# Kernel optimization log

Hardware: AMD Instinct MI355X
Metric: run time of the kernel (lower is better)

Reference implementation:

```python
import jax, jax.numpy as jnp
import numpy as np

N, C, H, W = 16, 256, 48, 96
S = 64   # num_s = 2*num_state_mid; also num_n = mids*mids = 64 (must match)
EPS = 1e-5


def setup_inputs() -> dict:
    key = jax.random.key(0)
    ks = jax.random.split(key, 11)
    sc = 0.05
    return {
        "x": jax.random.normal(ks[0], (N, C, H, W), jnp.float32),
        "edge": jax.random.normal(ks[1], (N, 2, H, W), jnp.float32),
        # conv_state: Conv2d(C, S, 1) with bias
        "Ws": jax.random.normal(ks[2], (S, C), jnp.float32) * sc,
        "bs": jax.random.normal(ks[3], (S,), jnp.float32) * sc,
        # conv_proj: Conv2d(C, S, 1) with bias
        "Wp": jax.random.normal(ks[4], (S, C), jnp.float32) * sc,
        "bp": jax.random.normal(ks[5], (S,), jnp.float32) * sc,
        # GCN conv1: Conv1d(num_n, num_n, 1, bias=False)
        "W1": jax.random.normal(ks[6], (S, S), jnp.float32) * sc,
        # GCN conv2: Conv1d(S, S, 1, bias=False)
        "W2": jax.random.normal(ks[7], (S, S), jnp.float32) * sc,
        # conv_extend: Conv2d(S, C, 1, bias=False)
        "We": jax.random.normal(ks[8], (C, S), jnp.float32) * sc,
        # BatchNorm2d(C) affine params (training-mode batch stats used in forward)
        "gamma": jnp.ones((C,), jnp.float32),
        "beta": jnp.zeros((C,), jnp.float32),
    }


def reference(x, edge, Ws, bs, Wp, bp, W1, W2, We, gamma, beta):
    n, c, h, w = x.shape
    s = Ws.shape[0]
    # edge softmax over channels, take class-1 probability map  -> (n,1,h,w)
    edge_g = jax.nn.softmax(edge, axis=1)[:, 1:2]

    # 1x1 convs as channel matmuls
    xs = jnp.einsum('oc,nchw->nohw', Ws, x) + bs[None, :, None, None]
    xs = xs.reshape(n, s, h * w)                        # (n,S,HW)
    xp = jnp.einsum('oc,nchw->nohw', Wp, x) + bp[None, :, None, None]
    # x_proj_region + x_proj_edge == xp * (1 + edge_gate)
    comb = (xp * (1.0 + edge_g)).reshape(n, s, h * w)
    comb = jax.nn.softmax(comb, axis=-1)                # softmax over spatial

    # project to graph space: (n,S,HW) @ (n,HW,S) -> (n,S,S)
    xn = jnp.einsum('nsk,ntk->nst', xs, comb)

    # GCN: conv1 over node dim (last axis mixes via W1), subtract, conv2 over state dim, relu
    hh = jnp.einsum('ij,nsj->nsi', W1, xn) - xn
    hh = jax.nn.relu(jnp.einsum('ij,njk->nik', W2, hh))

    # back-project: (n,S,S) @ (n,S,HW) -> (n,S,HW) -> (n,S,H,W)
    xr = jnp.einsum('nst,ntk->nsk', hh, comb).reshape(n, s, h, w)

    # conv_extend (no bias) then BatchNorm2d in training mode (biased batch var)
    ext = jnp.einsum('os,nshw->nohw', We, xr)
    mean = ext.mean(axis=(0, 2, 3), keepdims=True)
    var = ext.var(axis=(0, 2, 3), keepdims=True)
    bn = gamma[None, :, None, None] * (ext - mean) * jax.lax.rsqrt(var + EPS) \
         + beta[None, :, None, None]
    return x + bn
```

## Files before the change

### kernel.cpp

```cpp
#include <hip/hip_runtime.h>

#define HW 4608
#define NB 16
#define CC 256
#define SS 64
#define EPS 1e-5f
#define NSPLIT 24

typedef __attribute__((ext_vector_type(8))) short short8;
typedef __attribute__((ext_vector_type(4))) float f32x4;

__device__ __forceinline__ ushort f2bf(float f) {
    uint u = __float_as_uint(f);
    return (ushort)((u + 0x7FFFu + ((u >> 16) & 1u)) >> 16);
}
__device__ __forceinline__ float bf2f(ushort h) {
    return __uint_as_float(((uint)h) << 16);
}

__global__ __launch_bounds__(256) void k_wf(const float* __restrict__ Ws,
                                            const float* __restrict__ Wp,
                                            ushort* __restrict__ Wf) {
    int idx = blockIdx.x * 256 + threadIdx.x;
    int j = idx & 7, r = (idx >> 3) & 127, kq = (idx >> 10) & 3, cs = idx >> 12;
    int c = cs * 32 + kq * 8 + j;
    float v = (r < 64) ? Ws[r * CC + c] : Wp[(r - 64) * CC + c];
    Wf[idx] = f2bf(v);
}

__global__ __launch_bounds__(256) void k_proj(const float* __restrict__ x,
                                              const ushort* __restrict__ Wf,
                                              const float* __restrict__ bs,
                                              const float* __restrict__ bp,
                                              const float* __restrict__ edge,
                                              ushort* __restrict__ xsb,
                                              ushort* __restrict__ Eb,
                                              float* __restrict__ rsum) {
    __shared__ __align__(16) ushort Bl[32 * 64 * 8];
    int n = blockIdx.y, k0 = blockIdx.x * 64;
    int tid = threadIdx.x, lane = tid & 63, w = tid >> 6;
    int q = lane >> 4, li = lane & 15;
    const float* xb = x + (size_t)n * CC * HW + k0 + lane;
#pragma unroll
    for (int i = 0; i < 8; i++) {
        int kq = i * 4 + w;
        union { ushort u[8]; uint4 v; } tmp;
#pragma unroll
        for (int j = 0; j < 8; j++)
            tmp.u[j] = f2bf(xb[(size_t)(kq * 8 + j) * HW]);
        *(uint4*)&Bl[(kq * 64 + lane) * 8] = tmp.v;
    }
    __syncthreads();
    f32x4 acc[2][4] = {};
    uint4 afn[2];
#pragma unroll
    for (int mt = 0; mt < 2; mt++)
        afn[mt] = *(const uint4*)&Wf[((0 * 4 + q) * 128 + w * 32 + mt * 16 + li) * 8];
#pragma unroll
    for (int cs = 0; cs < 8; cs++) {
        short8 af[2];
        af[0] = *(short8*)&afn[0];
        af[1] = *(short8*)&afn[1];
        if (cs < 7) {
#pragma unroll
            for (int mt = 0; mt < 2; mt++)
                afn[mt] = *(const uint4*)&Wf[(((cs + 1) * 4 + q) * 128 + w * 32 + mt * 16 + li) * 8];
        }
        short8 bfr[4];
#pragma unroll
        for (int nt = 0; nt < 4; nt++) {
            uint4 t = *(const uint4*)&Bl[((cs * 4 + q) * 64 + nt * 16 + li) * 8];
            bfr[nt] = *(short8*)&t;
        }
#pragma unroll
        for (int mt = 0; mt < 2; mt++)
#pragma unroll
            for (int nt = 0; nt < 4; nt++)
                acc[mt][nt] = __builtin_amdgcn_mfma_f32_16x16x32_bf16(af[mt], bfr[nt], acc[mt][nt], 0, 0, 0);
    }
    if (w < 2) {
#pragma unroll
        for (int mt = 0; mt < 2; mt++) {
#pragma unroll
            for (int rr = 0; rr < 4; rr++) {
                int s = w * 32 + mt * 16 + q * 4 + rr;
                float bv = bs[s];
#pragma unroll
                for (int nt = 0; nt < 4; nt++) {
                    int col = k0 + nt * 16 + li;
                    xsb[((size_t)n * SS + s) * HW + col] = f2bf(acc[mt][nt][rr] + bv);
                }
            }
        }
    } else {
        float ga[4];
#pragma unroll
        for (int nt = 0; nt < 4; nt++) {
            int col = k0 + nt * 16 + li;
            float e0 = edge[((size_t)n * 2 + 0) * HW + col];
            float e1 = edge[((size_t)n * 2 + 1) * HW + col];
            ga[nt] = 1.f + 1.f / (1.f + __expf(e0 - e1));
        }
        float rp[2][4];
#pragma unroll
        for (int mt = 0; mt < 2; mt++) {
#pragma unroll
            for (int rr = 0; rr < 4; rr++) {
                int s = (w - 2) * 32 + mt * 16 + q * 4 + rr;
                float bv = bp[s];
                float sum = 0.f;
#pragma unroll
                for (int nt = 0; nt < 4; nt++) {
                    int col = k0 + nt * 16 + li;
                    float e = __expf((acc[mt][nt][rr] + bv) * ga[nt]);
                    sum += e;
                    Eb[((size_t)n * SS + s) * HW + col] = f2bf(e);
                }
                rp[mt][rr] = sum;
            }
        }
#pragma unroll
        for (int b = 1; b < 16; b <<= 1)
#pragma unroll
            for (int mt = 0; mt < 2; mt++)
#pragma unroll
                for (int rr = 0; rr < 4; rr++)
                    rp[mt][rr] += __shfl_xor(rp[mt][rr], b, 64);
        if (li == 0) {
#pragma unroll
            for (int mt = 0; mt < 2; mt++)
#pragma unroll
                for (int rr = 0; rr < 4; rr++)
                    atomicAdd(&rsum[n * SS + (w - 2) * 32 + mt * 16 + q * 4 + rr], rp[mt][rr]);
        }
    }
}

__global__ __launch_bounds__(256) void k_graph(const ushort* __restrict__ xsb,
                                               const ushort* __restrict__ Eb,
                                               float* __restrict__ Up,
                                               float* __restrict__ Pp) {
    int n = blockIdx.y, sp = blockIdx.x;
    int kbase = sp * (HW / NSPLIT);
    int tid = threadIdx.x, lane = tid & 63, w = tid >> 6;
    int q = lane >> 4, li = lane & 15;
    bool isP = w >= 2;
    int half = w & 1;
    const ushort* Arow = isP ? Eb : xsb;
    f32x4 acc[2][4] = {};
    for (int ks = 0; ks < (HW / NSPLIT) / 32; ks++) {
        int kb = kbase + ks * 32 + q * 8;
        short8 af[2], bfr[4];
#pragma unroll
        for (int mt = 0; mt < 2; mt++) {
            int s = half * 32 + mt * 16 + li;
            uint4 t = *(const uint4*)&Arow[((size_t)n * SS + s) * HW + kb];
            af[mt] = *(short8*)&t;
        }
#pragma unroll
        for (int nt = 0; nt < 4; nt++) {
            int tt = nt * 16 + li;
            uint4 t = *(const uint4*)&Eb[((size_t)n * SS + tt) * HW + kb];
            bfr[nt] = *(short8*)&t;
        }
#pragma unroll
        for (int mt = 0; mt < 2; mt++)
#pragma unroll
            for (int nt = 0; nt < 4; nt++)
                acc[mt][nt] = __builtin_amdgcn_mfma_f32_16x16x32_bf16(af[mt], bfr[nt], acc[mt][nt], 0, 0, 0);
    }
    float* dst = (isP ? Pp : Up) + ((size_t)sp * NB + n) * 4096;
#pragma unroll
    for (int mt = 0; mt < 2; mt++)
#pragma unroll
        for (int nt = 0; nt < 4; nt++)
#pragma unroll
            for (int rr = 0; rr < 4; rr++) {
                int row = half * 32 + mt * 16 + q * 4 + rr;
                int col = nt * 16 + li;
                dst[row * 64 + col] = acc[mt][nt][rr];
            }
}

__global__ __launch_bounds__(256) void k_red(const float* __restrict__ Up,
                                             const float* __restrict__ Pp,
                                             float* __restrict__ U,
                                             float* __restrict__ P) {
    int idx = blockIdx.x * 256 + threadIdx.x;
    const float* src = (idx < 16384) ? Up : Pp;
    float* dst = (idx < 16384) ? U : P;
    int o = (idx & 16383) * 4;
    f32x4 s = {};
    for (int sp = 0; sp < NSPLIT; sp++) {
        f32x4 v = *(const f32x4*)&src[(size_t)sp * 65536 + o];
        s += v;
    }
    *(f32x4*)&dst[o] = s;
}

__global__ __launch_bounds__(256) void k_gcn(const float* __restrict__ U,
                                             const float* __restrict__ rsum,
                                             const float* __restrict__ W1,
                                             const float* __restrict__ W2,
                                             const float* __restrict__ We,
                                             float* __restrict__ M,
                                             ushort* __restrict__ Mf) {
    __shared__ __align__(16) float A[64 * 68];
    __shared__ __align__(16) float B[64 * 68];
    __shared__ __align__(16) float Cb[64 * 68];
    __shared__ float rs[64];
    int n = blockIdx.x;
    int cc = blockIdx.y;
    int tid = threadIdx.x;
    int t0 = tid >> 4, t1 = tid & 15;
    if (tid < 64) rs[tid] = 1.0f / rsum[n * SS + tid];
    __syncthreads();
#pragma unroll
    for (int i = 0; i < 16; i++) {
        int idx = tid + i * 256;
        int r = idx >> 6, cth = idx & 63;
        A[cth * 68 + r] = U[n * 4096 + idx] * rs[cth];
        B[cth * 68 + r] = W1[idx];
    }
    __syncthreads();
    {
        float acc[4][4] = {};
        for (int j = 0; j < 64; j++) {
            float4 a4 = *(const float4*)&A[j * 68 + t0 * 4];
            float4 b4 = *(const float4*)&B[j * 68 + t1 * 4];
            float a[4] = {a4.x, a4.y, a4.z, a4.w};
            float b[4] = {b4.x, b4.y, b4.z, b4.w};
#pragma unroll
            for (int p = 0; p < 4; p++)
#pragma unroll
                for (int qq = 0; qq < 4; qq++) acc[p][qq] += a[p] * b[qq];
        }
#pragma unroll
        for (int p = 0; p < 4; p++)
#pragma unroll
            for (int qq = 0; qq < 4; qq++) {
                acc[p][qq] -= A[(t1 * 4 + qq) * 68 + (t0 * 4 + p)];
                Cb[(t0 * 4 + p) * 68 + t1 * 4 + qq] = acc[p][qq];
            }
    }
    __syncthreads();
#pragma unroll
    for (int i = 0; i < 16; i++) {
        int idx = tid + i * 256;
        int r = idx >> 6, cth = idx & 63;
        B[cth * 68 + r] = W2[idx];
    }
    __syncthreads();
    {
        float acc[4][4] = {};
        for (int j = 0; j < 64; j++) {
            float4 a4 = *(const float4*)&B[j * 68 + t0 * 4];
            float4 b4 = *(const float4*)&Cb[j * 68 + t1 * 4];
            float a[4] = {a4.x, a4.y, a4.z, a4.w};
            float b[4] = {b4.x, b4.y, b4.z, b4.w};
#pragma unroll
            for (int p = 0; p < 4; p++)
#pragma unroll
                for (int qq = 0; qq < 4; qq++) acc[p][qq] += a[p] * b[qq];
        }
        __syncthreads();
#pragma unroll
        for (int p = 0; p < 4; p++)
#pragma unroll
            for (int qq = 0; qq < 4; qq++)
                A[(t0 * 4 + p) * 68 + t1 * 4 + qq] = fmaxf(acc[p][qq], 0.f);
    }
    __syncthreads();
#pragma unroll
    for (int i = 0; i < 16; i++) {
        int idx = tid + i * 256;
        int c = idx >> 6, j = idx & 63;
        B[j * 68 + c] = We[(cc * 64 + c) * 64 + j];
    }
    __syncthreads();
    {
        float acc[4][4] = {};
        for (int j = 0; j < 64; j++) {
            float4 a4 = *(const float4*)&B[j * 68 + t0 * 4];
            float4 b4 = *(const float4*)&A[j * 68 + t1 * 4];
            float a[4] = {a4.x, a4.y, a4.z, a4.w};
            float b[4] = {b4.x, b4.y, b4.z, b4.w};
#pragma unroll
            for (int p = 0; p < 4; p++)
#pragma unroll
                for (int qq = 0; qq < 4; qq++) acc[p][qq] += a[p] * b[qq];
        }
#pragma unroll
        for (int p = 0; p < 4; p++) {
            int c = cc * 64 + t0 * 4 + p;
            float v[4];
#pragma unroll
            for (int qq = 0; qq < 4; qq++) v[qq] = acc[p][qq] * rs[t1 * 4 + qq];
            float4 st = {v[0], v[1], v[2], v[3]};
            *(float4*)&M[((size_t)n * CC + c) * 64 + t1 * 4] = st;
#pragma unroll
            for (int qq = 0; qq < 4; qq++) {
                int t = t1 * 4 + qq;
                Mf[(size_t)n * 16384 + ((t >> 3) * 256 + c) * 8 + (t & 7)] = f2bf(v[qq]);
            }
        }
    }
}

__global__ __launch_bounds__(256) void k_stats(const float* __restrict__ M,
                                               const float* __restrict__ P,
                                               const float* __restrict__ rsum,
                                               const float* __restrict__ gamma,
                                               const float* __restrict__ beta,
                                               float* __restrict__ sc,
                                               float* __restrict__ bi) {
    __shared__ float ms[NB][64];
    __shared__ float red[256];
    int c = blockIdx.x;
    int tid = threadIdx.x;
    for (int i = tid; i < NB * 64; i += 256) {
        int n = i >> 6, s = i & 63;
        ms[n][s] = M[((size_t)n * CC + c) * 64 + s];
    }
    __syncthreads();
    float qa = 0.f;
    for (int n = 0; n < NB; n++) {
        const float* Pn = P + n * 4096;
#pragma unroll
        for (int p = 0; p < 16; p++) {
            int e = p * 256 + tid;
            qa += ms[n][e >> 6] * ms[n][e & 63] * Pn[e];
        }
    }
    float sa = 0.f;
    for (int i = tid; i < NB * 64; i += 256) {
        int n = i >> 6, s = i & 63;
        sa += ms[n][s] * rsum[n * SS + s];
    }
    red[tid] = qa;
    __syncthreads();
    for (int off = 128; off > 0; off >>= 1) {
        if (tid < off) red[tid] += red[tid + off];
        __syncthreads();
    }
    float qtot = red[0];
    __syncthreads();
    red[tid] = sa;
    __syncthreads();
    for (int off = 128; off > 0; off >>= 1) {
        if (tid < off) red[tid] += red[tid + off];
        __syncthreads();
    }
    if (tid == 0) {
        float stot = red[0];
        const float invM = 1.0f / ((float)NB * (float)HW);
        float mean = stot * invM;
        float var = qtot * invM - mean * mean;
        float s = gamma[c] * rsqrtf(var + EPS);
        sc[c] = s;
        bi[c] = beta[c] - s * mean;
    }
}

__global__ __launch_bounds__(256) void k_out(const float* __restrict__ x,
                                             const ushort* __restrict__ Mf,
                                             const ushort* __restrict__ Eb,
                                             const float* __restrict__ sc,
                                             const float* __restrict__ bi,
                                             float* __restrict__ out) {
    __shared__ __align__(16) ushort Bl[8 * 64 * 8];
    int n = blockIdx.y, k0 = blockIdx.x * 64;
    int tid = threadIdx.x, lane = tid & 63, w = tid >> 6;
    int q = lane >> 4, li = lane & 15;
    {
        int nl = tid & 63, pr = tid >> 6;
#pragma unroll
        for (int kk = 0; kk < 2; kk++) {
            int kq = pr * 2 + kk;
            union { ushort u[8]; uint4 v; } tmp;
#pragma unroll
            for (int j = 0; j < 8; j++)
                tmp.u[j] = Eb[((size_t)n * SS + kq * 8 + j) * HW + k0 + nl];
            *(uint4*)&Bl[(kq * 64 + nl) * 8] = tmp.v;
        }
    }
    __syncthreads();
    f32x4 acc[4][4] = {};
#pragma unroll
    for (int ks = 0; ks < 2; ks++) {
        short8 af[4], bfr[4];
#pragma unroll
        for (int mt = 0; mt < 4; mt++) {
            int c = w * 64 + mt * 16 + li;
            uint4 t = *(const uint4*)&Mf[(size_t)n * 16384 + ((ks * 4 + q) * 256 + c) * 8];
            af[mt] = *(short8*)&t;
        }
#pragma unroll
        for (int nt = 0; nt < 4; nt++) {
            int nl = nt * 16 + li;
            uint4 t = *(const uint4*)&Bl[((ks * 4 + q) * 64 + nl) * 8];
            bfr[nt] = *(short8*)&t;
        }
#pragma unroll
        for (int mt = 0; mt < 4; mt++)
#pragma unroll
            for (int nt = 0; nt < 4; nt++)
                acc[mt][nt] = __builtin_amdgcn_mfma_f32_16x16x32_bf16(af[mt], bfr[nt], acc[mt][nt], 0, 0, 0);
    }
#pragma unroll
    for (int mt = 0; mt < 4; mt++) {
#pragma unroll
        for (int rr = 0; rr < 4; rr++) {
            int c = w * 64 + mt * 16 + q * 4 + rr;
            float s_ = sc[c], bv = bi[c];
            size_t base = ((size_t)n * CC + c) * HW + k0;
#pragma unroll
            for (int nt = 0; nt < 4; nt++) {
                int col = nt * 16 + li;
                out[base + col] = x[base + col] + s_ * acc[mt][nt][rr] + bv;
            }
        }
    }
}

extern "C" void kernel_launch(void* const* d_in, const int* in_sizes, int n_in,
                              void* d_out, int out_size, void* d_ws, size_t ws_size,
                              hipStream_t stream) {
    const float* x = (const float*)d_in[0];
    const float* edge = (const float*)d_in[1];
    const float* Ws = (const float*)d_in[2];
    const float* bs = (const float*)d_in[3];
    const float* Wp = (const float*)d_in[4];
    const float* bp = (const float*)d_in[5];
    const float* W1 = (const float*)d_in[6];
    const float* W2 = (const float*)d_in[7];
    const float* We = (const float*)d_in[8];
    const float* gamma = (const float*)d_in[9];
    const float* beta = (const float*)d_in[10];
    float* out = (float*)d_out;

    char* base = (char*)d_ws;
    ushort* Wf  = (ushort*)base;                    base += 65536;
    ushort* xsb = (ushort*)base;                    base += 9437184;
    ushort* Eb  = (ushort*)base;                    base += 9437184;
    float*  Up  = (float*)base;                     base += (size_t)NSPLIT * NB * 4096 * 4;
    float*  Pp  = (float*)base;                     base += (size_t)NSPLIT * NB * 4096 * 4;
    float*  U   = (float*)base;                     base += 262144;
    float*  P   = (float*)base;                     base += 262144;
    float*  rsum= (float*)base;                     base += 4096;
    float*  M   = (float*)base;                     base += 1048576;
    ushort* Mf  = (ushort*)base;                    base += 524288;
    float*  sc  = (float*)base;                     base += 1024;
    float*  bi  = (float*)base;                     base += 1024;

    hipMemsetAsync(rsum, 0, 1024 * sizeof(float), stream);
    k_wf<<<128, 256, 0, stream>>>(Ws, Wp, Wf);
    k_proj<<<dim3(72, NB), 256, 0, stream>>>(x, Wf, bs, bp, edge, xsb, Eb, rsum);
    k_graph<<<dim3(NSPLIT, NB), 256, 0, stream>>>(xsb, Eb, Up, Pp);
    k_red<<<128, 256, 0, stream>>>(Up, Pp, U, P);
    k_gcn<<<dim3(NB, 4), 256, 0, stream>>>(U, rsum, W1, W2, We, M, Mf);
    k_stats<<<256, 256, 0, stream>>>(M, P, rsum, gamma, beta, sc, bi);
    k_out<<<dim3(72, NB), 256, 0, stream>>>(x, Mf, Eb, sc, bi, out);
}
```

Measured before the change: 224.1 us.

## Pre-transpose x into bf16 spatial-major layout before projection GEMM

Adds a k_pack kernel that converts x to bf16 and transposes it through shared memory into an [n][HW][C] buffer. k_proj then loads its B tiles as contiguous 16-byte vectors instead of gathering eight strided fp32 values per lane. The intent is to cut the strided global loads and per-element conversion in k_proj. The cost is an extra full pass over x: it reads x and writes, then re-reads, a 37.7 MB bf16 copy. That buffer is aliased onto the later scratch buffers, so it depends on the workspace being large enough.

```diff
diff --git a/kernel.cpp b/kernel.cpp
--- a/kernel.cpp
+++ b/kernel.cpp
@@ -28,7 +28,42 @@
     Wf[idx] = f2bf(v);
 }
 
-__global__ __launch_bounds__(256) void k_proj(const float* __restrict__ x,
+__global__ __launch_bounds__(256) void k_pack(const float* __restrict__ x,
+                                              ushort* __restrict__ xTb) {
+    __shared__ ushort T[256][65];
+    int n = blockIdx.y;
+    int kt = blockIdx.x >> 2, ct = blockIdx.x & 3;
+    int k0 = kt * 256, c0 = ct * 64;
+    int tid = threadIdx.x;
+    const float* src = x + ((size_t)n * CC + c0) * HW + k0;
+#pragma unroll
+    for (int i = 0; i < 16; i++) {
+        int off = (i * 256 + tid) * 4;
+        int r = off >> 8;
+        int col = off & 255;
+        float4 v = *(const float4*)&src[(size_t)r * HW + col];
+        T[col + 0][r] = f2bf(v.x);
+        T[col + 1][r] = f2bf(v.y);
+        T[col + 2][r] = f2bf(v.z);
+        T[col + 3][r] = f2bf(v.w);
+    }
+    __syncthreads();
+    ushort* dst = xTb + ((size_t)n * HW + k0) * CC + c0;
+#pragma unroll
+    for (int i = 0; i < 16; i++) {
+        int off = (i * 256 + tid) * 4;
+        int kr = off >> 6;
+        int cc2 = off & 63;
+        ushort4 o;
+        o.x = T[kr][cc2 + 0];
+        o.y = T[kr][cc2 + 1];
+        o.z = T[kr][cc2 + 2];
+        o.w = T[kr][cc2 + 3];
+        *(ushort4*)&dst[(size_t)kr * CC + cc2] = o;
+    }
+}
+
+__global__ __launch_bounds__(256) void k_proj(const ushort* __restrict__ xTb,
                                               const ushort* __restrict__ Wf,
                                               const float* __restrict__ bs,
                                               const float* __restrict__ bp,
@@ -40,15 +75,13 @@
     int n = blockIdx.y, k0 = blockIdx.x * 64;
     int tid = threadIdx.x, lane = tid & 63, w = tid >> 6;
     int q = lane >> 4, li = lane & 15;
-    const float* xb = x + (size_t)n * CC * HW + k0 + lane;
+    const ushort* xtb = xTb + ((size_t)n * HW + k0) * CC;
+    int colS = tid & 63, kq0 = tid >> 6;
 #pragma unroll
     for (int i = 0; i < 8; i++) {
-        int kq = i * 4 + w;
-        union { ushort u[8]; uint4 v; } tmp;
-#pragma unroll
-        for (int j = 0; j < 8; j++)
-            tmp.u[j] = f2bf(xb[(size_t)(kq * 8 + j) * HW]);
-        *(uint4*)&Bl[(kq * 64 + lane) * 8] = tmp.v;
+        int kq = i * 4 + kq0;
+        uint4 t = *(const uint4*)&xtb[(size_t)colS * CC + kq * 8];
+        *(uint4*)&Bl[(kq * 64 + colS) * 8] = t;
     }
     __syncthreads();
     f32x4 acc[2][4] = {};
@@ -443,19 +476,22 @@
     ushort* Wf  = (ushort*)base;                    base += 65536;
     ushort* xsb = (ushort*)base;                    base += 9437184;
     ushort* Eb  = (ushort*)base;                    base += 9437184;
-    float*  Up  = (float*)base;                     base += (size_t)NSPLIT * NB * 4096 * 4;
-    float*  Pp  = (float*)base;                     base += (size_t)NSPLIT * NB * 4096 * 4;
-    float*  U   = (float*)base;                     base += 262144;
-    float*  P   = (float*)base;                     base += 262144;
     float*  rsum= (float*)base;                     base += 4096;
-    float*  M   = (float*)base;                     base += 1048576;
-    ushort* Mf  = (ushort*)base;                    base += 524288;
     float*  sc  = (float*)base;                     base += 1024;
     float*  bi  = (float*)base;                     base += 1024;
+    char* ovl = base;
+    ushort* xTb = (ushort*)ovl;
+    float*  Up  = (float*)ovl;                      ovl += (size_t)NSPLIT * NB * 4096 * 4;
+    float*  Pp  = (float*)ovl;                      ovl += (size_t)NSPLIT * NB * 4096 * 4;
+    float*  U   = (float*)ovl;                      ovl += 262144;
+    float*  P   = (float*)ovl;                      ovl += 262144;
+    float*  M   = (float*)ovl;                      ovl += 1048576;
+    ushort* Mf  = (ushort*)ovl;                     ovl += 524288;
 
     hipMemsetAsync(rsum, 0, 1024 * sizeof(float), stream);
     k_wf<<<128, 256, 0, stream>>>(Ws, Wp, Wf);
-    k_proj<<<dim3(72, NB), 256, 0, stream>>>(x, Wf, bs, bp, edge, xsb, Eb, rsum);
+    k_pack<<<dim3(72, NB), 256, 0, stream>>>(x, xTb);
+    k_proj<<<dim3(72, NB), 256, 0, stream>>>(xTb, Wf, bs, bp, edge, xsb, Eb, rsum);
     k_graph<<<dim3(NSPLIT, NB), 256, 0, stream>>>(xsb, Eb, Up, Pp);
     k_red<<<128, 256, 0, stream>>>(Up, Pp, U, P);
     k_gcn<<<dim3(NB, 4), 256, 0, stream>>>(U, rsum, W1, W2, We, M, Mf);
```

Result: slower. 245.9 us (+9.7%).

## Widen projection tiles with coalesced staging and replace split-K reduction with atomics

Applied to the files above, without the earlier changes.

k_proj now handles 256 spatial columns per block instead of 64. It streams x in 32-channel chunks through float4 coalesced loads into an LDS staging buffer, converts each chunk to bf16 fragments, and has each wave compute a 64x128 output tile. This replaces the old strided scalar loads and cuts the grid from 72 to 18 blocks per batch. Separately, k_graph now accumulates its split-K partials straight into U and P with atomicAdd, so the k_red kernel and its large partial buffers are gone, and U and P are zeroed by the existing memset. The trade-offs are fewer blocks (288 total) with higher register use in k_proj, atomic contention on U and P, and non-deterministic float summation order.

```diff
diff --git a/kernel.cpp b/kernel.cpp
--- a/kernel.cpp
+++ b/kernel.cpp
@@ -36,82 +36,88 @@
                                               ushort* __restrict__ xsb,
                                               ushort* __restrict__ Eb,
                                               float* __restrict__ rsum) {
-    __shared__ __align__(16) ushort Bl[32 * 64 * 8];
-    int n = blockIdx.y, k0 = blockIdx.x * 64;
+    __shared__ __align__(16) float  Sg[32 * 260];
+    __shared__ __align__(16) ushort Fr[4 * 256 * 8];
+    int n = blockIdx.y, k0 = blockIdx.x * 256;
     int tid = threadIdx.x, lane = tid & 63, w = tid >> 6;
     int q = lane >> 4, li = lane & 15;
-    const float* xb = x + (size_t)n * CC * HW + k0 + lane;
-#pragma unroll
-    for (int i = 0; i < 8; i++) {
-        int kq = i * 4 + w;
-        union { ushort u[8]; uint4 v; } tmp;
-#pragma unroll
-        for (int j = 0; j < 8; j++)
-            tmp.u[j] = f2bf(xb[(size_t)(kq * 8 + j) * HW]);
-        *(uint4*)&Bl[(kq * 64 + lane) * 8] = tmp.v;
-    }
-    __syncthreads();
-    f32x4 acc[2][4] = {};
-    uint4 afn[2];
-#pragma unroll
-    for (int mt = 0; mt < 2; mt++)
-        afn[mt] = *(const uint4*)&Wf[((0 * 4 + q) * 128 + w * 32 + mt * 16 + li) * 8];
-#pragma unroll
+    int wr = w >> 1, wc = w & 1;
+    const float* xb = x + (size_t)n * CC * HW + k0;
+    f32x4 acc[4][8] = {};
+    uint4 afn[4];
+#pragma unroll
+    for (int mt = 0; mt < 4; mt++)
+        afn[mt] = *(const uint4*)&Wf[((0 * 4 + q) * 128 + wr * 64 + mt * 16 + li) * 8];
+#pragma unroll 1
     for (int cs = 0; cs < 8; cs++) {
-        short8 af[2];
-        af[0] = *(short8*)&afn[0];
-        af[1] = *(short8*)&afn[1];
+#pragma unroll
+        for (int i = 0; i < 8; i++) {
+            int cl = i * 4 + w;
+            float4 v = *(const float4*)&xb[(size_t)(cs * 32 + cl) * HW + lane * 4];
+            *(float4*)&Sg[cl * 260 + lane * 4] = v;
+        }
+        __syncthreads();
+#pragma unroll
+        for (int i = 0; i < 4; i++) {
+            int col = (tid & 63) + 64 * i;
+            union { ushort u[8]; uint4 v; } tmp;
+#pragma unroll
+            for (int j = 0; j < 8; j++)
+                tmp.u[j] = f2bf(Sg[(w * 8 + j) * 260 + col]);
+            *(uint4*)&Fr[(w * 256 + col) * 8] = tmp.v;
+        }
+        __syncthreads();
+        short8 af[4];
+#pragma unroll
+        for (int mt = 0; mt < 4; mt++) af[mt] = *(short8*)&afn[mt];
         if (cs < 7) {
 #pragma unroll
-            for (int mt = 0; mt < 2; mt++)
-                afn[mt] = *(const uint4*)&Wf[(((cs + 1) * 4 + q) * 128 + w * 32 + mt * 16 + li) * 8];
-        }
-        short8 bfr[4];
-#pragma unroll
-        for (int nt = 0; nt < 4; nt++) {
-            uint4 t = *(const uint4*)&Bl[((cs * 4 + q) * 64 + nt * 16 + li) * 8];
-            bfr[nt] = *(short8*)&t;
-        }
-#pragma unroll
-        for (int mt = 0; mt < 2; mt++)
-#pragma unroll
-            for (int nt = 0; nt < 4; nt++)
-                acc[mt][nt] = __builtin_amdgcn_mfma_f32_16x16x32_bf16(af[mt], bfr[nt], acc[mt][nt], 0, 0, 0);
-    }
-    if (w < 2) {
-#pragma unroll
-        for (int mt = 0; mt < 2; mt++) {
+            for (int mt = 0; mt < 4; mt++)
+                afn[mt] = *(const uint4*)&Wf[(((cs + 1) * 4 + q) * 128 + wr * 64 + mt * 16 + li) * 8];
+        }
+#pragma unroll
+        for (int nt = 0; nt < 8; nt++) {
+            uint4 t = *(const uint4*)&Fr[(q * 256 + wc * 128 + nt * 16 + li) * 8];
+            short8 bf8 = *(short8*)&t;
+#pragma unroll
+            for (int mt = 0; mt < 4; mt++)
+                acc[mt][nt] = __builtin_amdgcn_mfma_f32_16x16x32_bf16(af[mt], bf8, acc[mt][nt], 0, 0, 0);
+        }
+    }
+    if (wr == 0) {
+#pragma unroll
+        for (int mt = 0; mt < 4; mt++) {
 #pragma unroll
             for (int rr = 0; rr < 4; rr++) {
-                int s = w * 32 + mt * 16 + q * 4 + rr;
+                int s = mt * 16 + q * 4 + rr;
                 float bv = bs[s];
 #pragma unroll
-                for (int nt = 0; nt < 4; nt++) {
-                    int col = k0 + nt * 16 + li;
+                for (int nt = 0; nt < 8; nt++) {
+                    int col = k0 + wc * 128 + nt * 16 + li;
                     xsb[((size_t)n * SS + s) * HW + col] = f2bf(acc[mt][nt][rr] + bv);
                 }
             }
         }
     } else {
-        float ga[4];
-#pragma unroll
-        for (int nt = 0; nt < 4; nt++) {
-            int col = k0 + nt * 16 + li;
+        float ga[8];
+#pragma unroll
+        for (int nt = 0; nt < 8; nt++) {
+            int col = k0 + wc * 128 + nt * 16 + li;
             float e0 = edge[((size_t)n * 2 + 0) * HW + col];
             float e1 = edge[((size_t)n * 2 + 1) * HW + col];
             ga[nt] = 1.f + 1.f / (1.f + __expf(e0 - e1));
         }
-        float rp[2][4];
-#pragma unroll
-        for (int mt = 0; mt < 2; mt++) {
+        float rp[4][4];
+#pragma unroll
+        for (int mt = 0; mt < 4; mt++) {
 #pragma unroll
             for (int rr = 0; rr < 4; rr++) {
-                int s = (w - 2) * 32 + mt * 16 + q * 4 + rr;
+                int s = mt * 16 + q * 4 + rr;
                 float bv = bp[s];
                 float sum = 0.f;
 #pragma unroll
-                for (int nt = 0; nt < 4; nt++) {
-                    int col = k0 + nt * 16 + li;
+                for (int nt = 0; nt < 8; nt++) {
+                    int col = k0 + wc * 128 + nt * 16 + li;
                     float e = __expf((acc[mt][nt][rr] + bv) * ga[nt]);
                     sum += e;
                     Eb[((size_t)n * SS + s) * HW + col] = f2bf(e);
@@ -122,24 +128,24 @@
 #pragma unroll
         for (int b = 1; b < 16; b <<= 1)
 #pragma unroll
-            for (int mt = 0; mt < 2; mt++)
+            for (int mt = 0; mt < 4; mt++)
 #pragma unroll
                 for (int rr = 0; rr < 4; rr++)
                     rp[mt][rr] += __shfl_xor(rp[mt][rr], b, 64);
         if (li == 0) {
 #pragma unroll
-            for (int mt = 0; mt < 2; mt++)
+            for (int mt = 0; mt < 4; mt++)
 #pragma unroll
                 for (int rr = 0; rr < 4; rr++)
-                    atomicAdd(&rsum[n * SS + (w - 2) * 32 + mt * 16 + q * 4 + rr], rp[mt][rr]);
+                    atomicAdd(&rsum[n * SS + mt * 16 + q * 4 + rr], rp[mt][rr]);
         }
     }
 }
 
 __global__ __launch_bounds__(256) void k_graph(const ushort* __restrict__ xsb,
                                                const ushort* __restrict__ Eb,
-                                               float* __restrict__ Up,
-                                               float* __restrict__ Pp) {
+                                               float* __restrict__ U,
+                                               float* __restrict__ P) {
     int n = blockIdx.y, sp = blockIdx.x;
     int kbase = sp * (HW / NSPLIT);
     int tid = threadIdx.x, lane = tid & 63, w = tid >> 6;
@@ -169,7 +175,7 @@
             for (int nt = 0; nt < 4; nt++)
                 acc[mt][nt] = __builtin_amdgcn_mfma_f32_16x16x32_bf16(af[mt], bfr[nt], acc[mt][nt], 0, 0, 0);
     }
-    float* dst = (isP ? Pp : Up) + ((size_t)sp * NB + n) * 4096;
+    float* dst = (isP ? P : U) + (size_t)n * 4096;
 #pragma unroll
     for (int mt = 0; mt < 2; mt++)
 #pragma unroll
@@ -178,24 +184,8 @@
             for (int rr = 0; rr < 4; rr++) {
                 int row = half * 32 + mt * 16 + q * 4 + rr;
                 int col = nt * 16 + li;
-                dst[row * 64 + col] = acc[mt][nt][rr];
-            }
-}
-
-__global__ __launch_bounds__(256) void k_red(const float* __restrict__ Up,
-                                             const float* __restrict__ Pp,
-                                             float* __restrict__ U,
-                                             float* __restrict__ P) {
-    int idx = blockIdx.x * 256 + threadIdx.x;
-    const float* src = (idx < 16384) ? Up : Pp;
-    float* dst = (idx < 16384) ? U : P;
-    int o = (idx & 16383) * 4;
-    f32x4 s = {};
-    for (int sp = 0; sp < NSPLIT; sp++) {
-        f32x4 v = *(const f32x4*)&src[(size_t)sp * 65536 + o];
-        s += v;
-    }
-    *(f32x4*)&dst[o] = s;
+                atomicAdd(&dst[row * 64 + col], acc[mt][nt][rr]);
+            }
 }
 
 __global__ __launch_bounds__(256) void k_gcn(const float* __restrict__ U,
@@ -443,21 +433,18 @@
     ushort* Wf  = (ushort*)base;                    base += 65536;
     ushort* xsb = (ushort*)base;                    base += 9437184;
     ushort* Eb  = (ushort*)base;                    base += 9437184;
-    float*  Up  = (float*)base;                     base += (size_t)NSPLIT * NB * 4096 * 4;
-    float*  Pp  = (float*)base;                     base += (size_t)NSPLIT * NB * 4096 * 4;
+    float*  rsum= (float*)base;                     base += 4096;
     float*  U   = (float*)base;                     base += 262144;
     float*  P   = (float*)base;                     base += 262144;
-    float*  rsum= (float*)base;                     base += 4096;
     float*  M   = (float*)base;                     base += 1048576;
     ushort* Mf  = (ushort*)base;                    base += 524288;
     float*  sc  = (float*)base;                     base += 1024;
     float*  bi  = (float*)base;                     base += 1024;
 
-    hipMemsetAsync(rsum, 0, 1024 * sizeof(float), stream);
+    hipMemsetAsync(rsum, 0, 4096 + 262144 + 262144, stream);
     k_wf<<<128, 256, 0, stream>>>(Ws, Wp, Wf);
-    k_proj<<<dim3(72, NB), 256, 0, stream>>>(x, Wf, bs, bp, edge, xsb, Eb, rsum);
-    k_graph<<<dim3(NSPLIT, NB), 256, 0, stream>>>(xsb, Eb, Up, Pp);
-    k_red<<<128, 256, 0, stream>>>(Up, Pp, U, P);
+    k_proj<<<dim3(18, NB), 256, 0, stream>>>(x, Wf, bs, bp, edge, xsb, Eb, rsum);
+    k_graph<<<dim3(NSPLIT, NB), 256, 0, stream>>>(xsb, Eb, U, P);
     k_gcn<<<dim3(NB, 4), 256, 0, stream>>>(U, rsum, W1, W2, We, M, Mf);
     k_stats<<<256, 256, 0, stream>>>(M, P, rsum, gamma, beta, sc, bi);
     k_out<<<dim3(72, NB), 256, 0, stream>>>(x, Mf, Eb, sc, bi, out);
```

Result: slower. 236.2 us (+5.4%).
